# Kernel optimization log

Hardware: AMD Instinct MI355X
Metric: run time of the kernel (lower is better)

Reference implementation:

```python
import jax, jax.numpy as jnp
import numpy as np

N, F, E = 50000, 128, 800000
H, C1, C2 = 4, 32, 32  # heads, channel_in, channel_out
LRELU_SLOPE = 0.2
LN_EPS = 1e-5


def _gat_conv(x, src, dst, W_src, W_dst, att_src, att_dst, bias, n, h, c):
    # x: [n, f_in]; src/dst: [e] edge endpoints (message j->i)
    xs = (x @ W_src).reshape(n, h, c)  # source-side transform
    xd = (x @ W_dst).reshape(n, h, c)  # dest-side transform
    a_s = jnp.einsum('nhc,hc->nh', xs, att_src)  # [n,h]
    a_d = jnp.einsum('nhc,hc->nh', xd, att_dst)
    e = jax.nn.leaky_relu(a_s[src] + a_d[dst], LRELU_SLOPE)  # [E,h]
    m = jax.lax.stop_gradient(jax.ops.segment_max(e, dst, num_segments=n))
    ee = jnp.exp(e - m[dst])
    denom = jax.ops.segment_sum(ee, dst, num_segments=n)
    alpha = ee / (denom[dst] + 1e-16)  # segment softmax over incoming edges
    out = jax.ops.segment_sum(xs[src] * alpha[:, :, None], dst, num_segments=n)
    return out.reshape(n, h * c) + bias


def _layer_norm(x, gamma, beta):
    mu = jnp.mean(x, axis=-1, keepdims=True)
    var = jnp.var(x, axis=-1, keepdims=True)
    return (x - mu) * jax.lax.rsqrt(var + LN_EPS) * gamma + beta


def setup_inputs() -> dict:
    key = jax.random.key(0)
    ks = jax.random.split(key, 16)
    hid = H * C1  # 128
    out_dim = H * C2  # 128

    def glorot(k, shape, fan_in):
        return jax.random.normal(k, shape, dtype=jnp.float32) / np.sqrt(fan_in)

    x = jax.random.normal(ks[0], (N, F), dtype=jnp.float32)
    edge_index = jax.random.randint(ks[1], (2, E), 0, N, dtype=jnp.int32)

    return {
        'x': x,
        'edge_index': edge_index,
        # conv1 (in F -> H*C1)
        'W1_src': glorot(ks[2], (F, H * C1), F),
        'W1_dst': glorot(ks[3], (F, H * C1), F),
        'att1_src': glorot(ks[4], (H, C1), C1),
        'att1_dst': glorot(ks[5], (H, C1), C1),
        'b1': jnp.zeros((H * C1,), jnp.float32),
        # lin1 skip (F -> hid)
        'Wl1': glorot(ks[6], (F, hid), F),
        'bl1': jnp.zeros((hid,), jnp.float32),
        # LayerNorm over hid
        'gamma': jnp.ones((hid,), jnp.float32),
        'beta': jnp.zeros((hid,), jnp.float32),
        # conv2 (hid -> H*C2)
        'W2_src': glorot(ks[7], (hid, H * C2), hid),
        'W2_dst': glorot(ks[8], (hid, H * C2), hid),
        'att2_src': glorot(ks[9], (H, C2), C2),
        'att2_dst': glorot(ks[10], (H, C2), C2),
        'b2': jnp.zeros((H * C2,), jnp.float32),
        # lin2 skip (hid -> out_dim)
        'Wl2': glorot(ks[11], (hid, out_dim), hid),
        'bl2': jnp.zeros((out_dim,), jnp.float32),
    }


def reference(x, edge_index, W1_src, W1_dst, att1_src, att1_dst, b1, Wl1, bl1,
              gamma, beta, W2_src, W2_dst, att2_src, att2_dst, b2, Wl2, bl2):
    src, dst = edge_index[0], edge_index[1]
    h = _gat_conv(x, src, dst, W1_src, W1_dst, att1_src, att1_dst, b1, N, H, C1) \
        + (x @ Wl1 + bl1)
    h = jax.nn.relu(_layer_norm(h, gamma, beta))
    out = _gat_conv(h, src, dst, W2_src, W2_dst, att2_src, att2_dst, b2, N, H, C2) \
        + (h @ Wl2 + bl2)
    return out
```

## Files before the change

### kernel.cpp

```cpp
#include <hip/hip_runtime.h>

#define N_NODES 50000
#define E_EDGES 800000
#define LRELU 0.2f
#define LN_EPS 1e-5f
#define NBUCK 98
#define BSHIFT 9

typedef short bf16x8 __attribute__((ext_vector_type(8)));
typedef float f32x4 __attribute__((ext_vector_type(4)));

__device__ __forceinline__ ushort f2bf(float f) {
    uint u = __float_as_uint(f);
    u += 0x7FFF + ((u >> 16) & 1);
    return (ushort)(u >> 16);
}
__device__ __forceinline__ float bflo(uint u) { return __uint_as_float(u << 16); }
__device__ __forceinline__ float bfhi(uint u) { return __uint_as_float(u & 0xFFFF0000u); }

__global__ __launch_bounds__(256) void bucket_count_kernel(
    const int* __restrict__ dst, int* __restrict__ bucketCnt, int e)
{
    __shared__ int lhist[NBUCK];
    int t = threadIdx.x;
    if (t < NBUCK) lhist[t] = 0;
    __syncthreads();
    int e0 = blockIdx.x * 2048;
    int count = min(2048, e - e0);
    #pragma unroll
    for (int q = 0; q < 8; ++q) {
        int li = t + q * 256;
        if (li < count) atomicAdd(&lhist[dst[e0 + li] >> BSHIFT], 1);
    }
    __syncthreads();
    if (t < NBUCK && lhist[t]) atomicAdd(&bucketCnt[t], lhist[t]);
}

__global__ __launch_bounds__(128) void bucket_scan_kernel(
    const int* __restrict__ bucketCnt, int* __restrict__ bucketBase,
    int* __restrict__ bucketCursor)
{
    __shared__ int ls[128];
    int t = threadIdx.x;
    int v = (t < NBUCK) ? bucketCnt[t] : 0;
    ls[t] = v;
    __syncthreads();
    #pragma unroll
    for (int off = 1; off < 128; off <<= 1) {
        int u = (t >= off) ? ls[t - off] : 0;
        __syncthreads();
        ls[t] += u;
        __syncthreads();
    }
    if (t < NBUCK) {
        int ex = ls[t] - v;
        bucketBase[t] = ex;
        bucketCursor[t] = ex;
    }
    if (t == NBUCK - 1) bucketBase[NBUCK] = ls[t];
}

__global__ __launch_bounds__(256) void bucket_scatter_kernel(
    const int* __restrict__ src, const int* __restrict__ dst,
    int* __restrict__ bucketCursor, uint* __restrict__ pairs, int e)
{
    __shared__ int lhist[128];
    __shared__ int lscan[NBUCK];
    __shared__ int lcur[NBUCK];
    __shared__ int lbase[NBUCK];
    __shared__ uint stageW[2048];
    __shared__ int  stageA[2048];
    int t = threadIdx.x;
    int e0 = blockIdx.x * 2048;
    int count = min(2048, e - e0);

    if (t < 128) lhist[t] = 0;
    if (t < NBUCK) lcur[t] = 0;
    __syncthreads();

    int  bb[8];
    uint pk[8];
    #pragma unroll
    for (int q = 0; q < 8; ++q) {
        int li = t + q * 256;
        if (li < count) {
            int d = dst[e0 + li];
            int s = src[e0 + li];
            bb[q] = d >> BSHIFT;
            pk[q] = (uint)s | ((uint)(d & 511) << 16);
            atomicAdd(&lhist[bb[q]], 1);
        } else bb[q] = -1;
    }
    __syncthreads();

    int orig = (t < 128) ? lhist[t] : 0;
    #pragma unroll
    for (int off = 1; off < 128; off <<= 1) {
        int u = 0;
        if (t < 128 && t >= off) u = lhist[t - off];
        __syncthreads();
        if (t < 128) lhist[t] += u;
        __syncthreads();
    }
    if (t < NBUCK) {
        lscan[t] = lhist[t] - orig;
        lbase[t] = orig ? atomicAdd(&bucketCursor[t], orig) : 0;
    }
    __syncthreads();

    #pragma unroll
    for (int q = 0; q < 8; ++q) {
        if (bb[q] >= 0) {
            int slot = lscan[bb[q]] + atomicAdd(&lcur[bb[q]], 1);
            stageW[slot] = pk[q];
            stageA[slot] = lbase[bb[q]] + (slot - lscan[bb[q]]);
        }
    }
    __syncthreads();

    #pragma unroll
    for (int q = 0; q < 8; ++q) {
        int li = t + q * 256;
        if (li < count) pairs[stageA[li]] = stageW[li];
    }
}

__global__ __launch_bounds__(512) void bucket_sort_kernel(
    const uint* __restrict__ pairs, const int* __restrict__ bucketBase,
    int* __restrict__ offs, ushort* __restrict__ srcSorted, int n, int e)
{
    __shared__ int cnt[512], cur[512], ls[512];
    int b = blockIdx.x, t = threadIdx.x;
    int base = bucketBase[b];
    int m = bucketBase[b + 1] - base;
    cnt[t] = 0; cur[t] = 0;
    __syncthreads();
    for (int i = t; i < m; i += 512)
        atomicAdd(&cnt[pairs[base + i] >> 16], 1);
    __syncthreads();
    int orig = cnt[t];
    ls[t] = orig;
    __syncthreads();
    #pragma unroll
    for (int off = 1; off < 512; off <<= 1) {
        int u = (t >= off) ? ls[t - off] : 0;
        __syncthreads();
        ls[t] += u;
        __syncthreads();
    }
    int excl = ls[t] - orig;
    int node = (b << BSHIFT) + t;
    if (node < n) offs[node] = base + excl;
    if (b == NBUCK - 1 && t == 0) offs[n] = e;
    cnt[t] = excl;
    __syncthreads();
    for (int i = t; i < m; i += 512) {
        uint w = pairs[base + i];
        int dl = w >> 16;
        int pos = cnt[dl] + atomicAdd(&cur[dl], 1);
        srcSorted[base + pos] = (ushort)(w & 0xFFFFu);
    }
}

__global__ __launch_bounds__(256) void prep_all_kernel(
    const float* __restrict__ W1s, const float* __restrict__ Wl1,
    const float* __restrict__ W1d, const float* __restrict__ a1s,
    const float* __restrict__ a1d,
    const float* __restrict__ W2s, const float* __restrict__ Wl2,
    const float* __restrict__ W2d, const float* __restrict__ a2s,
    const float* __restrict__ a2d,
    ushort* __restrict__ Wt, ushort* __restrict__ Watt)
{
    int t = threadIdx.x;
    if (blockIdx.x < 256) {
        int idx = blockIdx.x * 256 + t;
        int lw = idx >> 14, rem = idx & 16383;
        int nn = rem >> 7, k = rem & 127;
        const float* W = (lw == 0) ? W1s : (lw == 1) ? Wl1 : (lw == 2) ? W2s : Wl2;
        Wt[idx] = f2bf(W[k * 128 + nn]);
    } else {
        int L = blockIdx.x - 256;
        const float* Ws = L ? W2s : W1s;
        const float* Wd = L ? W2d : W1d;
        const float* as = L ? a2s : a1s;
        const float* adv = L ? a2d : a1d;
        #pragma unroll
        for (int q = 0; q < 8; ++q) {
            int e = q * 256 + t;
            int c = e >> 7, f = e & 127;
            float v = 0.f;
            if (c < 8) {
                const float* W  = (c < 4) ? Ws : Wd;
                const float* av = (c < 4) ? as : adv;
                int h = c & 3;
                #pragma unroll
                for (int j = 0; j < 32; ++j)
                    v += W[f * 128 + h * 32 + j] * av[h * 32 + j];
            }
            Watt[L * 2048 + c * 128 + f] = f2bf(v);
        }
    }
}

template <int LAYER>
__global__ __launch_bounds__(256) void gemm_fused_kernel(
    const float* __restrict__ Afp, const ushort* __restrict__ Abf,
    const ushort* __restrict__ Wt, const ushort* __restrict__ Watt,
    ushort* __restrict__ Cbf, float* __restrict__ a_sd, int n)
{
    __shared__ ushort Asb[64][136];
    __shared__ ushort Wsb[128][136];
    __shared__ ushort Attb[16][136];
    const int z = blockIdx.x;
    const int row0 = blockIdx.y * 64;
    const int tid = threadIdx.x;

    if (LAYER == 0) {
        #pragma unroll
        for (int i = 0; i < 8; ++i) {
            int idx = tid + i * 256;
            int r = idx >> 5, c4 = idx & 31;
            int grow = row0 + r;
            float4 v = make_float4(0.f, 0.f, 0.f, 0.f);
            if (grow < n) v = *(const float4*)(Afp + (size_t)grow * 128 + c4 * 4);
            ushort4 o;
            o.x = f2bf(v.x); o.y = f2bf(v.y); o.z = f2bf(v.z); o.w = f2bf(v.w);
            *(ushort4*)&Asb[r][c4 * 4] = o;
        }
    } else {
        #pragma unroll
        for (int i = 0; i < 4; ++i) {
            int c = tid + i * 256;
            int r = c >> 4, o = c & 15;
            int grow = row0 + r;
            uint4 v = make_uint4(0, 0, 0, 0);
            if (grow < n) v = *(const uint4*)(Abf + (size_t)grow * 128 + o * 8);
            *(uint4*)&Asb[r][o * 8] = v;
        }
    }
    {
        const ushort* Wz = Wt + (size_t)(LAYER * 2 + z) * 16384;
        #pragma unroll
        for (int i = 0; i < 8; ++i) {
            int c = tid + i * 256;
            int r = c >> 4, o = c & 15;
            uint4 v = *(const uint4*)(Wz + r * 128 + o * 8);
            *(uint4*)&Wsb[r][o * 8] = v;
        }
    }
    if (z == 0) {
        int r = tid >> 4, o = tid & 15;
        uint4 v = *(const uint4*)(Watt + LAYER * 2048 + r * 128 + o * 8);
        *(uint4*)&Attb[r][o * 8] = v;
    }
    __syncthreads();

    const int w = tid >> 6, lane = tid & 63;
    const int wm = w >> 1, wn = w & 1;
    const int l15 = lane & 15, lg = lane >> 4;
    const bool doAtt = (z == 0) && (wn == 0);

    f32x4 acc[2][4];
    f32x4 accA[2];
    #pragma unroll
    for (int m = 0; m < 2; ++m) {
        accA[m] = (f32x4){0.f, 0.f, 0.f, 0.f};
        #pragma unroll
        for (int j = 0; j < 4; ++j)
            acc[m][j] = (f32x4){0.f, 0.f, 0.f, 0.f};
    }

    #pragma unroll
    for (int ks = 0; ks < 4; ++ks) {
        const int k0 = ks * 32 + 4 * lg;
        bf16x8 af[2], bfr[4];
        #pragma unroll
        for (int m = 0; m < 2; ++m) {
            const ushort* p = &Asb[wm * 32 + m * 16 + l15][k0];
            ushort4 lo = *(const ushort4*)p;
            ushort4 hi = *(const ushort4*)(p + 16);
            bf16x8 a;
            a[0] = (short)lo.x; a[1] = (short)lo.y; a[2] = (short)lo.z; a[3] = (short)lo.w;
            a[4] = (short)hi.x; a[5] = (short)hi.y; a[6] = (short)hi.z; a[7] = (short)hi.w;
            af[m] = a;
        }
        #pragma unroll
        for (int j = 0; j < 4; ++j) {
            const ushort* p = &Wsb[wn * 64 + j * 16 + l15][k0];
            ushort4 lo = *(const ushort4*)p;
            ushort4 hi = *(const ushort4*)(p + 16);
            bf16x8 b;
            b[0] = (short)lo.x; b[1] = (short)lo.y; b[2] = (short)lo.z; b[3] = (short)lo.w;
            b[4] = (short)hi.x; b[5] = (short)hi.y; b[6] = (short)hi.z; b[7] = (short)hi.w;
            bfr[j] = b;
        }
        #pragma unroll
        for (int m = 0; m < 2; ++m)
            #pragma unroll
            for (int j = 0; j < 4; ++j)
                acc[m][j] = __builtin_amdgcn_mfma_f32_16x16x32_bf16(
                    af[m], bfr[j], acc[m][j], 0, 0, 0);
        if (doAtt) {
            const ushort* p = &Attb[l15][k0];
            ushort4 lo = *(const ushort4*)p;
            ushort4 hi = *(const ushort4*)(p + 16);
            bf16x8 b;
            b[0] = (short)lo.x; b[1] = (short)lo.y; b[2] = (short)lo.z; b[3] = (short)lo.w;
            b[4] = (short)hi.x; b[5] = (short)hi.y; b[6] = (short)hi.z; b[7] = (short)hi.w;
            #pragma unroll
            for (int m = 0; m < 2; ++m)
                accA[m] = __builtin_amdgcn_mfma_f32_16x16x32_bf16(
                    af[m], b, accA[m], 0, 0, 0);
        }
    }

    #pragma unroll
    for (int m = 0; m < 2; ++m)
        #pragma unroll
        for (int j = 0; j < 4; ++j)
            #pragma unroll
            for (int r = 0; r < 4; ++r) {
                int grow = row0 + wm * 32 + m * 16 + lg * 4 + r;
                if (grow < n)
                    Cbf[(size_t)grow * 256 + z * 128 + wn * 64 + j * 16 + l15] =
                        f2bf(acc[m][j][r]);
            }
    if (doAtt && l15 < 8) {
        #pragma unroll
        for (int m = 0; m < 2; ++m)
            #pragma unroll
            for (int r = 0; r < 4; ++r) {
                int grow = row0 + wm * 32 + m * 16 + lg * 4 + r;
                if (grow < n) a_sd[(size_t)grow * 8 + l15] = accA[m][r];
            }
    }
}

template <int MODE>
__global__ __launch_bounds__(256) void aggregate_fused_kernel(
    const ushort* __restrict__ srcSorted, const int* __restrict__ offs,
    const ushort* __restrict__ bufbf,
    const float* __restrict__ a_sd,
    const float* __restrict__ bias_a, const float* __restrict__ bias_l,
    const float* __restrict__ gamma, const float* __restrict__ beta,
    ushort* __restrict__ hbf, float* __restrict__ out, int n)
{
    int node = (blockIdx.x * blockDim.x + threadIdx.x) >> 6;
    int lane = threadIdx.x & 63;
    if (node >= n) return;
    int beg = offs[node], end = offs[node + 1];
    const int j = lane >> 4;
    const int g = lane & 15;
    const int h = g >> 2;
    const int je = lane & 3, he = lane >> 2;

    float adh = 0.f;
    if (lane < 16) adh = a_sd[(size_t)node * 8 + 4 + he];

    float acc[8] = {};
    float denp = 0.f;

    for (int t = beg; t < end; t += 4) {
        int s = 0; float ee = 0.f;
        if (lane < 16) {
            int idx = t + je;
            int ic = (idx < end) ? idx : (end - 1);
            s = srcSorted[ic];
            float as = a_sd[(size_t)s * 8 + he];
            float e = as + adh;
            e = (e > 0.f) ? e : LRELU * e;
            ee = (idx < end) ? __expf(e) : 0.f;
            denp += ee;
        }
        int   sq  = __shfl(s, j);
        float eeq = __shfl(ee, h * 4 + j);
        uint4 xv = *(const uint4*)(bufbf + (size_t)sq * 256 + g * 8);
        acc[0] = fmaf(eeq, bflo(xv.x), acc[0]);
        acc[1] = fmaf(eeq, bfhi(xv.x), acc[1]);
        acc[2] = fmaf(eeq, bflo(xv.y), acc[2]);
        acc[3] = fmaf(eeq, bfhi(xv.y), acc[3]);
        acc[4] = fmaf(eeq, bflo(xv.z), acc[4]);
        acc[5] = fmaf(eeq, bfhi(xv.z), acc[5]);
        acc[6] = fmaf(eeq, bflo(xv.w), acc[6]);
        acc[7] = fmaf(eeq, bfhi(xv.w), acc[7]);
    }

    #pragma unroll
    for (int c = 0; c < 8; ++c) {
        acc[c] += __shfl_xor(acc[c], 16);
        acc[c] += __shfl_xor(acc[c], 32);
    }
    denp += __shfl_xor(denp, 1);
    denp += __shfl_xor(denp, 2);

    if (lane < 16) {
        float inv = 1.f / (denp + 1e-16f);
        uint4 sk = *(const uint4*)(bufbf + (size_t)node * 256 + 128 + g * 8);
        float4 ba0 = *(const float4*)(bias_a + g * 8);
        float4 ba1 = *(const float4*)(bias_a + g * 8 + 4);
        float4 bl0 = *(const float4*)(bias_l + g * 8);
        float4 bl1 = *(const float4*)(bias_l + g * 8 + 4);
        float v[8];
        v[0] = acc[0] * inv + bflo(sk.x) + ba0.x + bl0.x;
        v[1] = acc[1] * inv + bfhi(sk.x) + ba0.y + bl0.y;
        v[2] = acc[2] * inv + bflo(sk.y) + ba0.z + bl0.z;
        v[3] = acc[3] * inv + bfhi(sk.y) + ba0.w + bl0.w;
        v[4] = acc[4] * inv + bflo(sk.z) + ba1.x + bl1.x;
        v[5] = acc[5] * inv + bfhi(sk.z) + ba1.y + bl1.y;
        v[6] = acc[6] * inv + bflo(sk.w) + ba1.z + bl1.z;
        v[7] = acc[7] * inv + bfhi(sk.w) + ba1.w + bl1.w;

        if (MODE == 0) {
            float sum = 0.f, sq = 0.f;
            #pragma unroll
            for (int c = 0; c < 8; ++c) { sum += v[c]; sq += v[c] * v[c]; }
            #pragma unroll
            for (int off = 1; off < 16; off <<= 1) {
                sum += __shfl_xor(sum, off);
                sq  += __shfl_xor(sq, off);
            }
            float mu = sum * (1.f / 128.f);
            float var = sq * (1.f / 128.f) - mu * mu;
            float rs = rsqrtf(var + LN_EPS);
            float4 gm0 = *(const float4*)(gamma + g * 8);
            float4 gm1 = *(const float4*)(gamma + g * 8 + 4);
            float4 bt0 = *(const float4*)(beta + g * 8);
            float4 bt1 = *(const float4*)(beta + g * 8 + 4);
            float o[8];
            o[0] = fmaxf((v[0] - mu) * rs * gm0.x + bt0.x, 0.f);
            o[1] = fmaxf((v[1] - mu) * rs * gm0.y + bt0.y, 0.f);
            o[2] = fmaxf((v[2] - mu) * rs * gm0.z + bt0.z, 0.f);
            o[3] = fmaxf((v[3] - mu) * rs * gm0.w + bt0.w, 0.f);
            o[4] = fmaxf((v[4] - mu) * rs * gm1.x + bt1.x, 0.f);
            o[5] = fmaxf((v[5] - mu) * rs * gm1.y + bt1.y, 0.f);
            o[6] = fmaxf((v[6] - mu) * rs * gm1.z + bt1.z, 0.f);
            o[7] = fmaxf((v[7] - mu) * rs * gm1.w + bt1.w, 0.f);
            uint4 st;
            st.x = (uint)f2bf(o[0]) | ((uint)f2bf(o[1]) << 16);
            st.y = (uint)f2bf(o[2]) | ((uint)f2bf(o[3]) << 16);
            st.z = (uint)f2bf(o[4]) | ((uint)f2bf(o[5]) << 16);
            st.w = (uint)f2bf(o[6]) | ((uint)f2bf(o[7]) << 16);
            *(uint4*)(hbf + (size_t)node * 128 + g * 8) = st;
        } else {
            *(float4*)(out + (size_t)node * 128 + g * 8) =
                make_float4(v[0], v[1], v[2], v[3]);
            *(float4*)(out + (size_t)node * 128 + g * 8 + 4) =
                make_float4(v[4], v[5], v[6], v[7]);
        }
    }
}

extern "C" void kernel_launch(void* const* d_in, const int* in_sizes, int n_in,
                              void* d_out, int out_size, void* d_ws, size_t ws_size,
                              hipStream_t stream) {
    const float* x       = (const float*)d_in[0];
    const int*   ei      = (const int*)d_in[1];
    const int*   src     = ei;
    const int*   dst     = ei + E_EDGES;
    const float* W1_src  = (const float*)d_in[2];
    const float* W1_dst  = (const float*)d_in[3];
    const float* att1_s  = (const float*)d_in[4];
    const float* att1_d  = (const float*)d_in[5];
    const float* b1      = (const float*)d_in[6];
    const float* Wl1     = (const float*)d_in[7];
    const float* bl1     = (const float*)d_in[8];
    const float* gamma   = (const float*)d_in[9];
    const float* beta    = (const float*)d_in[10];
    const float* W2_src  = (const float*)d_in[11];
    const float* W2_dst  = (const float*)d_in[12];
    const float* att2_s  = (const float*)d_in[13];
    const float* att2_d  = (const float*)d_in[14];
    const float* b2      = (const float*)d_in[15];
    const float* Wl2     = (const float*)d_in[16];
    const float* bl2     = (const float*)d_in[17];
    float* out = (float*)d_out;

    char* p = (char*)d_ws;
    float* a_sd        = (float*)p;      p += (size_t)N_NODES * 8 * 4;
    int* offs          = (int*)p;        p += (size_t)(N_NODES + 1) * 4;
    int* bucketCnt     = (int*)p;        p += (NBUCK) * 4;
    int* bucketBase    = (int*)p;        p += (NBUCK + 1) * 4;
    int* bucketCursor  = (int*)p;        p += (NBUCK + 1) * 4;
    uint* pairs        = (uint*)p;       p += (size_t)E_EDGES * 4;
    ushort* hbf        = (ushort*)p;     p += (size_t)N_NODES * 128 * 2;
    ushort* bufbf      = (ushort*)p;     p += (size_t)N_NODES * 256 * 2;
    ushort* Wt         = (ushort*)p;     p += (size_t)4 * 16384 * 2;
    ushort* Watt       = (ushort*)p;     p += (size_t)2 * 2048 * 2;
    ushort* srcSorted  = (ushort*)p;     p += (size_t)E_EDGES * 2;

    dim3 ggrid(2, (N_NODES + 63) / 64);
    int edge_blocks = (E_EDGES + 2047) / 2048;
    int wave_grid   = (N_NODES + 3) / 4;

    hipMemsetAsync(bucketCnt, 0, NBUCK * sizeof(int), stream);
    bucket_count_kernel<<<edge_blocks, 256, 0, stream>>>(dst, bucketCnt, E_EDGES);
    bucket_scan_kernel<<<1, 128, 0, stream>>>(bucketCnt, bucketBase, bucketCursor);
    bucket_scatter_kernel<<<edge_blocks, 256, 0, stream>>>(src, dst, bucketCursor, pairs, E_EDGES);
    bucket_sort_kernel<<<NBUCK, 512, 0, stream>>>(pairs, bucketBase, offs, srcSorted, N_NODES, E_EDGES);

    prep_all_kernel<<<258, 256, 0, stream>>>(
        W1_src, Wl1, W1_dst, att1_s, att1_d,
        W2_src, Wl2, W2_dst, att2_s, att2_d, Wt, Watt);

    gemm_fused_kernel<0><<<ggrid, 256, 0, stream>>>(x, nullptr, Wt, Watt, bufbf, a_sd, N_NODES);
    aggregate_fused_kernel<0><<<wave_grid, 256, 0, stream>>>(
        srcSorted, offs, bufbf, a_sd, b1, bl1, gamma, beta, hbf, nullptr, N_NODES);

    gemm_fused_kernel<1><<<ggrid, 256, 0, stream>>>(nullptr, hbf, Wt, Watt, bufbf, a_sd, N_NODES);
    aggregate_fused_kernel<1><<<wave_grid, 256, 0, stream>>>(
        srcSorted, offs, bufbf, a_sd, b2, bl2, nullptr, nullptr, nullptr, out, N_NODES);
}
```

Measured before the change: 325.6 us.

## Use fixed-capacity edge buckets, stage GEMM stores via LDS, unroll aggregation

```diff
diff --git a/kernel.cpp b/kernel.cpp
--- a/kernel.cpp
+++ b/kernel.cpp
@@ -6,6 +6,7 @@
 #define LN_EPS 1e-5f
 #define NBUCK 98
 #define BSHIFT 9
+#define BCAP 9216
 
 typedef short bf16x8 __attribute__((ext_vector_type(8)));
 typedef float f32x4 __attribute__((ext_vector_type(4)));
@@ -17,48 +18,6 @@
 }
 __device__ __forceinline__ float bflo(uint u) { return __uint_as_float(u << 16); }
 __device__ __forceinline__ float bfhi(uint u) { return __uint_as_float(u & 0xFFFF0000u); }
-
-__global__ __launch_bounds__(256) void bucket_count_kernel(
-    const int* __restrict__ dst, int* __restrict__ bucketCnt, int e)
-{
-    __shared__ int lhist[NBUCK];
-    int t = threadIdx.x;
-    if (t < NBUCK) lhist[t] = 0;
-    __syncthreads();
-    int e0 = blockIdx.x * 2048;
-    int count = min(2048, e - e0);
-    #pragma unroll
-    for (int q = 0; q < 8; ++q) {
-        int li = t + q * 256;
-        if (li < count) atomicAdd(&lhist[dst[e0 + li] >> BSHIFT], 1);
-    }
-    __syncthreads();
-    if (t < NBUCK && lhist[t]) atomicAdd(&bucketCnt[t], lhist[t]);
-}
-
-__global__ __launch_bounds__(128) void bucket_scan_kernel(
-    const int* __restrict__ bucketCnt, int* __restrict__ bucketBase,
-    int* __restrict__ bucketCursor)
-{
-    __shared__ int ls[128];
-    int t = threadIdx.x;
-    int v = (t < NBUCK) ? bucketCnt[t] : 0;
-    ls[t] = v;
-    __syncthreads();
-    #pragma unroll
-    for (int off = 1; off < 128; off <<= 1) {
-        int u = (t >= off) ? ls[t - off] : 0;
-        __syncthreads();
-        ls[t] += u;
-        __syncthreads();
-    }
-    if (t < NBUCK) {
-        int ex = ls[t] - v;
-        bucketBase[t] = ex;
-        bucketCursor[t] = ex;
-    }
-    if (t == NBUCK - 1) bucketBase[NBUCK] = ls[t];
-}
 
 __global__ __launch_bounds__(256) void bucket_scatter_kernel(
     const int* __restrict__ src, const int* __restrict__ dst,
@@ -104,7 +63,7 @@
     }
     if (t < NBUCK) {
         lscan[t] = lhist[t] - orig;
-        lbase[t] = orig ? atomicAdd(&bucketCursor[t], orig) : 0;
+        lbase[t] = t * BCAP + (orig ? atomicAdd(&bucketCursor[t], orig) : 0);
     }
     __syncthreads();
 
@@ -126,13 +85,14 @@
 }
 
 __global__ __launch_bounds__(512) void bucket_sort_kernel(
-    const uint* __restrict__ pairs, const int* __restrict__ bucketBase,
-    int* __restrict__ offs, ushort* __restrict__ srcSorted, int n, int e)
+    const uint* __restrict__ pairs, const int* __restrict__ bucketCursor,
+    int* __restrict__ offs, ushort* __restrict__ degs,
+    ushort* __restrict__ srcSorted, int n)
 {
     __shared__ int cnt[512], cur[512], ls[512];
     int b = blockIdx.x, t = threadIdx.x;
-    int base = bucketBase[b];
-    int m = bucketBase[b + 1] - base;
+    int base = b * BCAP;
+    int m = bucketCursor[b];
     cnt[t] = 0; cur[t] = 0;
     __syncthreads();
     for (int i = t; i < m; i += 512)
@@ -150,8 +110,10 @@
     }
     int excl = ls[t] - orig;
     int node = (b << BSHIFT) + t;
-    if (node < n) offs[node] = base + excl;
-    if (b == NBUCK - 1 && t == 0) offs[n] = e;
+    if (node < n) {
+        offs[node] = base + excl;
+        degs[node] = (ushort)orig;
+    }
     cnt[t] = excl;
     __syncthreads();
     for (int i = t; i < m; i += 512) {
@@ -314,17 +276,6 @@
         }
     }
 
-    #pragma unroll
-    for (int m = 0; m < 2; ++m)
-        #pragma unroll
-        for (int j = 0; j < 4; ++j)
-            #pragma unroll
-            for (int r = 0; r < 4; ++r) {
-                int grow = row0 + wm * 32 + m * 16 + lg * 4 + r;
-                if (grow < n)
-                    Cbf[(size_t)grow * 256 + z * 128 + wn * 64 + j * 16 + l15] =
-                        f2bf(acc[m][j][r]);
-            }
     if (doAtt && l15 < 8) {
         #pragma unroll
         for (int m = 0; m < 2; ++m)
@@ -334,11 +285,34 @@
                 if (grow < n) a_sd[(size_t)grow * 8 + l15] = accA[m][r];
             }
     }
+
+    __syncthreads();
+    ushort (*Cs)[136] = (ushort(*)[136])&Asb[0][0];
+    #pragma unroll
+    for (int m = 0; m < 2; ++m)
+        #pragma unroll
+        for (int j = 0; j < 4; ++j)
+            #pragma unroll
+            for (int r = 0; r < 4; ++r)
+                Cs[wm * 32 + m * 16 + lg * 4 + r][wn * 64 + j * 16 + l15] =
+                    f2bf(acc[m][j][r]);
+    __syncthreads();
+    #pragma unroll
+    for (int i = 0; i < 4; ++i) {
+        int u4 = tid + i * 256;
+        int r = u4 >> 4, c8 = u4 & 15;
+        int grow = row0 + r;
+        if (grow < n) {
+            uint4 v = *(const uint4*)&Cs[r][c8 * 8];
+            *(uint4*)(Cbf + (size_t)grow * 256 + z * 128 + c8 * 8) = v;
+        }
+    }
 }
 
 template <int MODE>
 __global__ __launch_bounds__(256) void aggregate_fused_kernel(
     const ushort* __restrict__ srcSorted, const int* __restrict__ offs,
+    const ushort* __restrict__ degs,
     const ushort* __restrict__ bufbf,
     const float* __restrict__ a_sd,
     const float* __restrict__ bias_a, const float* __restrict__ bias_l,
@@ -348,41 +322,53 @@
     int node = (blockIdx.x * blockDim.x + threadIdx.x) >> 6;
     int lane = threadIdx.x & 63;
     if (node >= n) return;
-    int beg = offs[node], end = offs[node + 1];
+    int beg = offs[node];
+    int end = beg + degs[node];
     const int j = lane >> 4;
     const int g = lane & 15;
     const int h = g >> 2;
-    const int je = lane & 3, he = lane >> 2;
+    const int he2 = (lane >> 3) & 3;
 
     float adh = 0.f;
-    if (lane < 16) adh = a_sd[(size_t)node * 8 + 4 + he];
+    if (lane < 32) adh = a_sd[(size_t)node * 8 + 4 + he2];
 
     float acc[8] = {};
     float denp = 0.f;
 
-    for (int t = beg; t < end; t += 4) {
+    for (int t = beg; t < end; t += 8) {
         int s = 0; float ee = 0.f;
-        if (lane < 16) {
-            int idx = t + je;
+        if (lane < 32) {
+            int idx = t + (lane & 7);
             int ic = (idx < end) ? idx : (end - 1);
             s = srcSorted[ic];
-            float as = a_sd[(size_t)s * 8 + he];
+            float as = a_sd[(size_t)s * 8 + he2];
             float e = as + adh;
             e = (e > 0.f) ? e : LRELU * e;
             ee = (idx < end) ? __expf(e) : 0.f;
             denp += ee;
         }
-        int   sq  = __shfl(s, j);
-        float eeq = __shfl(ee, h * 4 + j);
-        uint4 xv = *(const uint4*)(bufbf + (size_t)sq * 256 + g * 8);
-        acc[0] = fmaf(eeq, bflo(xv.x), acc[0]);
-        acc[1] = fmaf(eeq, bfhi(xv.x), acc[1]);
-        acc[2] = fmaf(eeq, bflo(xv.y), acc[2]);
-        acc[3] = fmaf(eeq, bfhi(xv.y), acc[3]);
-        acc[4] = fmaf(eeq, bflo(xv.z), acc[4]);
-        acc[5] = fmaf(eeq, bfhi(xv.z), acc[5]);
-        acc[6] = fmaf(eeq, bflo(xv.w), acc[6]);
-        acc[7] = fmaf(eeq, bfhi(xv.w), acc[7]);
+        int   sA  = __shfl(s, j);
+        int   sB  = __shfl(s, j + 4);
+        float eeA = __shfl(ee, h * 8 + j);
+        float eeB = __shfl(ee, h * 8 + j + 4);
+        uint4 xA = *(const uint4*)(bufbf + (size_t)sA * 256 + g * 8);
+        uint4 xB = *(const uint4*)(bufbf + (size_t)sB * 256 + g * 8);
+        acc[0] = fmaf(eeA, bflo(xA.x), acc[0]);
+        acc[1] = fmaf(eeA, bfhi(xA.x), acc[1]);
+        acc[2] = fmaf(eeA, bflo(xA.y), acc[2]);
+        acc[3] = fmaf(eeA, bfhi(xA.y), acc[3]);
+        acc[4] = fmaf(eeA, bflo(xA.z), acc[4]);
+        acc[5] = fmaf(eeA, bfhi(xA.z), acc[5]);
+        acc[6] = fmaf(eeA, bflo(xA.w), acc[6]);
+        acc[7] = fmaf(eeA, bfhi(xA.w), acc[7]);
+        acc[0] = fmaf(eeB, bflo(xB.x), acc[0]);
+        acc[1] = fmaf(eeB, bfhi(xB.x), acc[1]);
+        acc[2] = fmaf(eeB, bflo(xB.y), acc[2]);
+        acc[3] = fmaf(eeB, bfhi(xB.y), acc[3]);
+        acc[4] = fmaf(eeB, bflo(xB.z), acc[4]);
+        acc[5] = fmaf(eeB, bfhi(xB.z), acc[5]);
+        acc[6] = fmaf(eeB, bflo(xB.w), acc[6]);
+        acc[7] = fmaf(eeB, bfhi(xB.w), acc[7]);
     }
 
     #pragma unroll
@@ -392,9 +378,11 @@
     }
     denp += __shfl_xor(denp, 1);
     denp += __shfl_xor(denp, 2);
+    denp += __shfl_xor(denp, 4);
+    float den = __shfl(denp, (g >> 2) * 8);
 
     if (lane < 16) {
-        float inv = 1.f / (denp + 1e-16f);
+        float inv = 1.f / (den + 1e-16f);
         uint4 sk = *(const uint4*)(bufbf + (size_t)node * 256 + 128 + g * 8);
         float4 ba0 = *(const float4*)(bias_a + g * 8);
         float4 ba1 = *(const float4*)(bias_a + g * 8 + 4);
@@ -477,26 +465,23 @@
 
     char* p = (char*)d_ws;
     float* a_sd        = (float*)p;      p += (size_t)N_NODES * 8 * 4;
-    int* offs          = (int*)p;        p += (size_t)(N_NODES + 1) * 4;
-    int* bucketCnt     = (int*)p;        p += (NBUCK) * 4;
-    int* bucketBase    = (int*)p;        p += (NBUCK + 1) * 4;
-    int* bucketCursor  = (int*)p;        p += (NBUCK + 1) * 4;
-    uint* pairs        = (uint*)p;       p += (size_t)E_EDGES * 4;
+    int* offs          = (int*)p;        p += (size_t)N_NODES * 4;
+    int* bucketCursor  = (int*)p;        p += 128 * 4;
+    uint* pairs        = (uint*)p;       p += (size_t)NBUCK * BCAP * 4;
+    ushort* degs       = (ushort*)p;     p += (size_t)N_NODES * 2;
     ushort* hbf        = (ushort*)p;     p += (size_t)N_NODES * 128 * 2;
     ushort* bufbf      = (ushort*)p;     p += (size_t)N_NODES * 256 * 2;
     ushort* Wt         = (ushort*)p;     p += (size_t)4 * 16384 * 2;
     ushort* Watt       = (ushort*)p;     p += (size_t)2 * 2048 * 2;
-    ushort* srcSorted  = (ushort*)p;     p += (size_t)E_EDGES * 2;
+    ushort* srcSorted  = (ushort*)p;     p += (size_t)NBUCK * BCAP * 2;
 
     dim3 ggrid(2, (N_NODES + 63) / 64);
     int edge_blocks = (E_EDGES + 2047) / 2048;
     int wave_grid   = (N_NODES + 3) / 4;
 
-    hipMemsetAsync(bucketCnt, 0, NBUCK * sizeof(int), stream);
-    bucket_count_kernel<<<edge_blocks, 256, 0, stream>>>(dst, bucketCnt, E_EDGES);
-    bucket_scan_kernel<<<1, 128, 0, stream>>>(bucketCnt, bucketBase, bucketCursor);
+    hipMemsetAsync(bucketCursor, 0, NBUCK * sizeof(int), stream);
     bucket_scatter_kernel<<<edge_blocks, 256, 0, stream>>>(src, dst, bucketCursor, pairs, E_EDGES);
-    bucket_sort_kernel<<<NBUCK, 512, 0, stream>>>(pairs, bucketBase, offs, srcSorted, N_NODES, E_EDGES);
+    bucket_sort_kernel<<<NBUCK, 512, 0, stream>>>(pairs, bucketCursor, offs, degs, srcSorted, N_NODES);
 
     prep_all_kernel<<<258, 256, 0, stream>>>(
         W1_src, Wl1, W1_dst, att1_s, att1_d,
@@ -504,9 +489,9 @@
 
     gemm_fused_kernel<0><<<ggrid, 256, 0, stream>>>(x, nullptr, Wt, Watt, bufbf, a_sd, N_NODES);
     aggregate_fused_kernel<0><<<wave_grid, 256, 0, stream>>>(
-        srcSorted, offs, bufbf, a_sd, b1, bl1, gamma, beta, hbf, nullptr, N_NODES);
+        srcSorted, offs, degs, bufbf, a_sd, b1, bl1, gamma, beta, hbf, nullptr, N_NODES);
 
     gemm_fused_kernel<1><<<ggrid, 256, 0, stream>>>(nullptr, hbf, Wt, Watt, bufbf, a_sd, N_NODES);
     aggregate_fused_kernel<1><<<wave_grid, 256, 0, stream>>>(
-        srcSorted, offs, bufbf, a_sd, b2, bl2, nullptr, nullptr, nullptr, out, N_NODES);
-}
+        srcSorted, offs, degs, bufbf, a_sd, b2, bl2, nullptr, nullptr, nullptr, out, N_NODES);
+}
```

Result: faster. 293.4 us (-9.9%).
